# Optimization experiments

Measured on AMD Instinct MI355X. Metric: run time of the kernel, lower is better.

Reference implementation:

```python
import jax, jax.numpy as jnp
import numpy as np
from jax import lax

NUM_MELS = 80
NQ = 256          # num_quants
WIN = 1024
HOP = 256
K_UP = 800        # upsample kernel
PAD_UP = K_UP + 4 * HOP - WIN   # = 800
RC = 120          # residual_channels
SC = 240          # skip_channels
KC = 2            # causal kernel
NB = 16           # num blocks
DILS = [1, 2, 4, 8, 16, 32, 64, 128] * 2
DN = ('NCH', 'OIH', 'NCH')


def conv1x1(x, w, b):
    # x: [B,C,T], w: [O,C], b: [O]
    return jnp.einsum('bct,oc->bot', x, w) + b[None, :, None]


def causal_conv(x, w, b, d):
    # x: [B,RC,T], w: [2RC,RC,KC], left-pad by d*(KC-1) -> causal, same length
    y = lax.conv_general_dilated(x, w, (1,), [(d * (KC - 1), 0)],
                                 rhs_dilation=(d,), dimension_numbers=DN)
    return y + b[None, :, None]


def setup_inputs() -> dict:
    key = jax.random.key(0)
    ks = jax.random.split(key, 20)
    s = 0.05
    n = jax.random.normal
    return {
        'waveforms': n(ks[0], (1, 40960), jnp.float32),
        'melspecs': n(ks[1], (1, NUM_MELS, 160), jnp.float32),
        # ConvTranspose-equivalent upsample weight, stored as direct conv weight [O,I,K]
        'up_w': s * n(ks[2], (NUM_MELS, NUM_MELS, K_UP), jnp.float32),
        'up_b': jnp.zeros((NUM_MELS,), jnp.float32),
        'in_w': s * n(ks[3], (RC, 1), jnp.float32),
        'in_b': jnp.zeros((RC,), jnp.float32),
        'blk_causal_w': s * n(ks[4], (NB, 2 * RC, RC, KC), jnp.float32),
        'blk_causal_b': jnp.zeros((NB, 2 * RC), jnp.float32),
        'blk_cond_w': s * n(ks[5], (NB, 2 * RC, NUM_MELS), jnp.float32),
        'blk_cond_b': jnp.zeros((NB, 2 * RC), jnp.float32),
        'blk_skip_w': s * n(ks[6], (NB, SC, RC), jnp.float32),
        'blk_skip_b': jnp.zeros((NB, SC), jnp.float32),
        'blk_res_w': s * n(ks[7], (NB, RC, RC), jnp.float32),
        'blk_res_b': jnp.zeros((NB, RC), jnp.float32),
        'h1_w': s * n(ks[8], (NQ, SC), jnp.float32),
        'h1_b': jnp.zeros((NQ,), jnp.float32),
        'h2_w': s * n(ks[9], (NQ, NQ), jnp.float32),
        'h2_b': jnp.zeros((NQ,), jnp.float32),
    }


def _forward(waveforms, melspecs, up_w, up_b, in_w, in_b,
             blk_causal_w, blk_causal_b, blk_cond_w, blk_cond_b,
             blk_skip_w, blk_skip_b, blk_res_w, blk_res_b,
             h1_w, h1_b, h2_w, h2_b):
    # ConvTranspose1d(stride=HOP, padding=PAD_UP) as lhs-dilated conv:
    # out_len = (F-1)*HOP + K_UP - 2*PAD_UP
    cond = lax.conv_general_dilated(
        melspecs, up_w, (1,), [(K_UP - 1 - PAD_UP, K_UP - 1 - PAD_UP)],
        lhs_dilation=(HOP,), dimension_numbers=DN) + up_b[None, :, None]
    L = min(waveforms.shape[-1], cond.shape[-1])
    wav = waveforms[..., :L]
    cond = cond[..., :L]

    res = conv1x1(wav[:, None, :], in_w, in_b)          # [B,RC,L]
    skip_sum = jnp.zeros((res.shape[0], SC, L), res.dtype)
    for i, d in enumerate(DILS):
        z = causal_conv(res, blk_causal_w[i], blk_causal_b[i], d) \
            + conv1x1(cond, blk_cond_w[i], blk_cond_b[i])  # [B,2RC,L]
        h = jnp.tanh(z[:, :RC]) * jax.nn.sigmoid(z[:, RC:])
        skip_sum = skip_sum + conv1x1(h, blk_skip_w[i], blk_skip_b[i])
        res = res + conv1x1(h, blk_res_w[i], blk_res_b[i])

    x = jax.nn.relu(skip_sum)
    x = jax.nn.relu(conv1x1(x, h1_w, h1_b))
    logits = conv1x1(x, h2_w, h2_b)                      # [B,NQ,L]
    return logits


def reference(waveforms, melspecs, up_w, up_b, in_w, in_b,
              blk_causal_w, blk_causal_b, blk_cond_w, blk_cond_b,
              blk_skip_w, blk_skip_b, blk_res_w, blk_res_b,
              h1_w, h1_b, h2_w, h2_b):
    return _forward(waveforms, melspecs, up_w, up_b, in_w, in_b,
                    blk_causal_w, blk_causal_b, blk_cond_w, blk_cond_b,
                    blk_skip_w, blk_skip_b, blk_res_w, blk_res_b,
                    h1_w, h1_b, h2_w, h2_b)
```

## Files before the change

### kernel.cpp

```cpp
#include <hip/hip_runtime.h>

#define L_LEN 39904
#define NT 624
#define RCH 120
#define SCH 240
#define CMEL 80
#define NQO 256
#define NBLK 16
#define KUP 800

typedef unsigned short u16;
typedef __attribute__((ext_vector_type(8))) short short8;
typedef __attribute__((ext_vector_type(4))) float f32x4;

#define MFMA(a, b, c) __builtin_amdgcn_mfma_f32_16x16x32_bf16((a), (b), (c), 0, 0, 0)

__device__ __forceinline__ u16 f2bf(float f) {
    unsigned u = __float_as_uint(f);
    u += 0x7FFFu + ((u >> 16) & 1u);
    return (u16)(u >> 16);
}
__device__ __forceinline__ unsigned pack2(float a, float b) {
    return (unsigned)f2bf(a) | ((unsigned)f2bf(b) << 16);
}
__device__ __forceinline__ float b16tof(u16 h) {
    return __uint_as_float((unsigned)h << 16);
}
__device__ __forceinline__ float gate(float a, float b) {
    float ea = __expf(2.f * a);
    float th = 1.f - 2.f * __builtin_amdgcn_rcpf(ea + 1.f);
    float sg = __builtin_amdgcn_rcpf(1.f + __expf(-b));
    return th * sg;
}

constexpr size_t O_CONDT = 0;
constexpr size_t O_RESA  = O_CONDT + 7023104;
constexpr size_t O_RESB  = O_RESA + 19153920;
constexpr size_t O_SKIP  = O_RESB + 19153920;
constexpr size_t O_ZFRAG = O_SKIP + 19153920;
constexpr size_t O_SKF   = O_ZFRAG + 2621440;
constexpr size_t O_RF    = O_SKF + 1048576;
constexpr size_t O_H1F   = O_RF + 524288;
constexpr size_t O_H2F   = O_H1F + 131072;
constexpr size_t O_UPF   = O_H2F + 131072;
constexpr size_t O_ZB    = O_UPF + 13107200;
constexpr size_t O_SKB   = O_ZB + 16384;

constexpr size_t H2_CONDT = 0;
constexpr size_t H2_RESF  = 7023104;
constexpr size_t H2_BFA   = H2_RESF + 19153920;
constexpr size_t H2_BFB   = H2_BFA + 9576960;
constexpr size_t H2_ZFRAG = H2_BFB + 9576960;
constexpr size_t H2_SKF   = H2_ZFRAG + 2621440;
constexpr size_t H2_RF    = H2_SKF + 1048576;
constexpr size_t H2_H1F   = H2_RF + 524288;
constexpr size_t H2_H2F   = H2_H1F + 131072;
constexpr size_t H2_ZB    = H2_H2F + 131072;
constexpr size_t H2_SKBS  = H2_ZB + 16384;
constexpr size_t H2_HALL  = H2_SKBS + 16384;
constexpr size_t H_BYTES  = (size_t)NBLK * L_LEN * 120 * 2;
constexpr size_t UPF_BYTES = 13107200;
constexpr size_t NEED_H = H2_HALL + (H_BYTES > UPF_BYTES ? H_BYTES : UPF_BYTES);

__global__ void k_prep_zfrag(const float* __restrict__ bc_w, const float* __restrict__ bq_w,
                             u16* __restrict__ dst) {
    int i = blockIdx.x * 256 + threadIdx.x;
    if (i >= NBLK * 10 * 16 * 512) return;
    int jj = i & 7, lane = (i >> 3) & 63, mt = (i >> 9) & 15;
    int rest = i >> 13, ks = rest % 10, blk = rest / 10;
    int m = mt * 16 + (lane & 15);
    int k = ks * 32 + ((lane >> 4) << 3) + jj;
    float v = 0.f;
    if (m < 240) {
        int o = (m & 1) ? (m >> 1) + 120 : (m >> 1);
        if (k < 120)       v = bc_w[((size_t)(blk * 240 + o) * 120 + k) * 2 + 0];
        else if (k < 240)  v = bc_w[((size_t)(blk * 240 + o) * 120 + (k - 120)) * 2 + 1];
        else               v = bq_w[(size_t)(blk * 240 + o) * 80 + (k - 240)];
    }
    dst[i] = f2bf(v);
}
__global__ void k_prep_skfrag(const float* __restrict__ bs_w, u16* __restrict__ dst) {
    int i = blockIdx.x * 256 + threadIdx.x;
    if (i >= NBLK * 4 * 16 * 512) return;
    int jj = i & 7, lane = (i >> 3) & 63, mt = (i >> 9) & 15;
    int rest = i >> 13, ks = rest & 3, blk = rest >> 2;
    int m = mt * 16 + (lane & 15);
    int k = ks * 32 + ((lane >> 4) << 3) + jj;
    float v = (m < 240 && k < 120) ? bs_w[(size_t)(blk * 240 + m) * 120 + k] : 0.f;
    dst[i] = f2bf(v);
}
__global__ void k_prep_rfrag(const float* __restrict__ br_w, u16* __restrict__ dst) {
    int i = blockIdx.x * 256 + threadIdx.x;
    if (i >= NBLK * 4 * 8 * 512) return;
    int jj = i & 7, lane = (i >> 3) & 63, mt = (i >> 9) & 7;
    int rest = i >> 12, ks = rest & 3, blk = rest >> 2;
    int m = mt * 16 + (lane & 15);
    int k = ks * 32 + ((lane >> 4) << 3) + jj;
    float v = (m < 120 && k < 120) ? br_w[(size_t)(blk * 120 + m) * 120 + k] : 0.f;
    dst[i] = f2bf(v);
}
__global__ void k_prep_h1frag(const float* __restrict__ h1_w, u16* __restrict__ dst) {
    int i = blockIdx.x * 256 + threadIdx.x;
    if (i >= 8 * 16 * 512) return;
    int jj = i & 7, lane = (i >> 3) & 63, mt = (i >> 9) & 15, ks = i >> 13;
    int m = mt * 16 + (lane & 15);
    int k = ks * 32 + ((lane >> 4) << 3) + jj;
    float v = (k < 240) ? h1_w[(size_t)m * 240 + k] : 0.f;
    dst[i] = f2bf(v);
}
__global__ void k_prep_h2frag(const float* __restrict__ h2_w, u16* __restrict__ dst) {
    int i = blockIdx.x * 256 + threadIdx.x;
    if (i >= 8 * 16 * 512) return;
    int jj = i & 7, lane = (i >> 3) & 63, mt = (i >> 9) & 15, ks = i >> 13;
    int m = mt * 16 + (lane & 15);
    int k = ks * 32 + ((lane >> 4) << 3) + jj;
    dst[i] = f2bf(h2_w[(size_t)m * 256 + k]);
}
__global__ void k_prep_upfrag(const float* __restrict__ up_w, u16* __restrict__ dst) {
    int i = blockIdx.x * 256 + threadIdx.x;
    if (i >= 256 * 10 * 5 * 512) return;
    int jj = i & 7, lane = (i >> 3) & 63;
    int rest = i >> 9;
    int mt = rest % 5; rest /= 5;
    int ks = rest % 10; int p = rest / 10;
    int m = mt * 16 + (lane & 15);
    int k = ks * 32 + ((lane >> 4) << 3) + jj;
    int c = k >> 2, j = k & 3;
    int r = (256 - ((p + 1) & 255)) & 255;
    int kk = r + 256 * j;
    float v = (m < 80 && kk < KUP) ? up_w[((size_t)m * 80 + c) * KUP + kk] : 0.f;
    dst[i] = f2bf(v);
}
__global__ void k_prep_zbias(const float* __restrict__ bc_b, const float* __restrict__ bq_b,
                             float* __restrict__ dst) {
    int i = blockIdx.x * 256 + threadIdx.x;
    if (i >= NBLK * 256) return;
    int m = i & 255, blk = i >> 8;
    float v = 0.f;
    if (m < 240) {
        int o = (m & 1) ? (m >> 1) + 120 : (m >> 1);
        v = bc_b[blk * 240 + o] + bq_b[blk * 240 + o];
    }
    dst[i] = v;
}
__global__ void k_prep_skbias(const float* __restrict__ bs_b, float* __restrict__ dst) {
    int i = blockIdx.x * 256 + threadIdx.x;
    if (i >= NBLK * 240) return;
    dst[i] = bs_b[i];
}
__global__ void k_prep_skbsum(const float* __restrict__ bs_b, float* __restrict__ dst) {
    int m = blockIdx.x * 256 + threadIdx.x;
    if (m >= 240) return;
    float s = 0.f;
    for (int i = 0; i < NBLK; i++) s += bs_b[i * 240 + m];
    dst[m] = s;
}
__global__ void k_res_initT(const float* __restrict__ wav, const float* __restrict__ in_w,
                            const float* __restrict__ in_b, float* __restrict__ resT) {
    int i = blockIdx.x * 256 + threadIdx.x;
    if (i >= L_LEN * RCH) return;
    int t = i / RCH, c = i % RCH;
    resT[i] = wav[t] * in_w[c] + in_b[c];
}
__global__ void k_res_initTb(const float* __restrict__ wav, const float* __restrict__ in_w,
                             const float* __restrict__ in_b, u16* __restrict__ resB) {
    int i = blockIdx.x * 256 + threadIdx.x;
    if (i >= L_LEN * RCH) return;
    int t = i / RCH, c = i % RCH;
    resB[i] = f2bf(wav[t] * in_w[c] + in_b[c]);
}

__global__ __launch_bounds__(256) void k_up(const float* __restrict__ mel,
        const u16* __restrict__ upf, const float* __restrict__ up_b,
        u16* __restrict__ condT) {
    __shared__ u16 s_ms[64 * 328];
    const int tid = threadIdx.x, l = tid & 63, w = tid >> 6;
    const int quad = l >> 4, tloc = l & 15;
    const int p = blockIdx.x, s0 = blockIdx.y * 64;
    for (int rr = 0; rr < 16; rr++) {
        int tt = w + 4 * rr;
        int sg = s0 + tt;
        #pragma unroll
        for (int base = 0; base < 320; base += 64) {
            int ck = base + l;
            int c = ck >> 2, j = ck & 3;
            int mi = 1 + j + sg;
            float v = (mi < 160) ? mel[c * 160 + mi] : 0.f;
            s_ms[tt * 328 + ck] = f2bf(v);
        }
    }
    __syncthreads();
    f32x4 acc[2][4];
    #pragma unroll
    for (int i = 0; i < 2; i++)
        #pragma unroll
        for (int n = 0; n < 4; n++) acc[i][n] = (f32x4){0.f, 0.f, 0.f, 0.f};
    const int nmt = (w == 0) ? 2 : 1;
    int mts[2]; mts[0] = w; mts[1] = 4;
    for (int ks = 0; ks < 10; ks++) {
        short8 b[4];
        int k0 = ks * 32 + quad * 8;
        #pragma unroll
        for (int n = 0; n < 4; n++)
            b[n] = *(const short8*)&s_ms[(n * 16 + tloc) * 328 + k0];
        const short8* ap = (const short8*)(upf) + ((size_t)p * 10 + ks) * 5 * 64;
        for (int i = 0; i < nmt; i++) {
            short8 a = ap[mts[i] * 64 + l];
            #pragma unroll
            for (int n = 0; n < 4; n++) acc[i][n] = MFMA(a, b[n], acc[i][n]);
        }
    }
    for (int i = 0; i < nmt; i++) {
        int o_base = mts[i] * 16 + quad * 4;
        float4 ub = *(const float4*)(up_b + o_base);
        float bb[4] = {ub.x, ub.y, ub.z, ub.w};
        #pragma unroll
        for (int n = 0; n < 4; n++) {
            int sg = s0 + n * 16 + tloc;
            int t = p + 256 * sg;
            if (t < L_LEN) {
                #pragma unroll
                for (int r = 0; r < 4; r++)
                    condT[(size_t)t * 88 + o_base + r] = f2bf(acc[i][n][r] + bb[r]);
            }
        }
    }
}

__global__ __launch_bounds__(512, 4) void k_block(
        const u16* __restrict__ condT, const float* __restrict__ resT_in,
        float* __restrict__ resT_out, u16* __restrict__ skipT,
        const u16* __restrict__ zfrag, const u16* __restrict__ skfrag,
        const u16* __restrict__ rfrag, const float* __restrict__ zbias,
        const float* __restrict__ skbias, const float* __restrict__ resb,
        int blk, int dil, int first) {
    __shared__ u16 s_x[64 * 328];
    u16* s_h = s_x;
    const int tid = threadIdx.x, l = tid & 63, w = tid >> 6;
    const int quad = l >> 4, tloc = l & 15;
    const int t0 = blockIdx.x * 64;
    const short8* zap = (const short8*)(zfrag) + (size_t)blk * 10 * 16 * 64;
    short8 a_cur[2], a_nxt[2];
    #pragma unroll
    for (int i = 0; i < 2; i++) a_cur[i] = zap[(size_t)(w * 2 + i) * 64 + l];
    for (int rr = 0; rr < 8; rr++) {
        int tt = w + 8 * rr;
        int tg = t0 + tt, tp = tg - dil;
        if (l < 60) {
            float2 pv = make_float2(0.f, 0.f), cv = make_float2(0.f, 0.f);
            if (tp >= 0 && tp < L_LEN) pv = *(const float2*)(resT_in + (size_t)tp * 120 + 2 * l);
            if (tg < L_LEN)            cv = *(const float2*)(resT_in + (size_t)tg * 120 + 2 * l);
            *(unsigned*)&s_x[tt * 328 + 2 * l]       = pack2(pv.x, pv.y);
// ... 86 lines not shown
            ra_n = rap[((size_t)(ks + 1) * 8 + w) * 64 + l];
        }
        short8 b[4];
        int k0 = ks * 32 + quad * 8;
        #pragma unroll
        for (int n = 0; n < 4; n++)
            b[n] = *(const short8*)&s_h[(n * 16 + tloc) * 136 + k0];
        #pragma unroll
        for (int i = 0; i < 2; i++)
            #pragma unroll
            for (int n = 0; n < 4; n++) sacc[i][n] = MFMA(sa_c[i], b[n], sacc[i][n]);
        #pragma unroll
        for (int n = 0; n < 4; n++) racc[n] = MFMA(ra_c, b[n], racc[n]);
        #pragma unroll
        for (int i = 0; i < 2; i++) sa_c[i] = sa_n[i];
        ra_c = ra_n;
    }
    #pragma unroll
    for (int i = 0; i < 2; i++) {
        int m_base = (w * 2 + i) * 16 + quad * 4;
        if (m_base >= 240) continue;
        float4 sb4 = *(const float4*)(skbias + blk * 240 + m_base);
        #pragma unroll
        for (int n = 0; n < 4; n++) {
            int t = t0 + n * 16 + tloc;
            if (t >= L_LEN) continue;
            float x0 = sacc[i][n][0] + sb4.x;
            float x1 = sacc[i][n][1] + sb4.y;
            float x2 = sacc[i][n][2] + sb4.z;
            float x3 = sacc[i][n][3] + sb4.w;
            if (!first) {
                uint2 pv = skp[i][n];
                x0 += b16tof((u16)(pv.x & 0xFFFF));
                x1 += b16tof((u16)(pv.x >> 16));
                x2 += b16tof((u16)(pv.y & 0xFFFF));
                x3 += b16tof((u16)(pv.y >> 16));
            }
            uint2 ov;
            ov.x = pack2(x0, x1);
            ov.y = pack2(x2, x3);
            *(uint2*)(skipT + (size_t)t * 240 + m_base) = ov;
        }
    }
    {
        int m_base = w * 16 + quad * 4;
        if (m_base < 120) {
            float4 rb4 = *(const float4*)(resb + blk * 120 + m_base);
            #pragma unroll
            for (int n = 0; n < 4; n++) {
                int t = t0 + n * 16 + tloc;
                if (t >= L_LEN) continue;
                float4 cur = *(const float4*)(resT_in + (size_t)t * 120 + m_base);
                float4 o;
                o.x = cur.x + racc[n][0] + rb4.x;
                o.y = cur.y + racc[n][1] + rb4.y;
                o.z = cur.z + racc[n][2] + rb4.z;
                o.w = cur.w + racc[n][3] + rb4.w;
                *(float4*)(resT_out + (size_t)t * 120 + m_base) = o;
            }
        }
    }
}

__global__ __launch_bounds__(512, 4) void k_block_h4(
        const u16* __restrict__ condT,
        const u16* __restrict__ bfIn, u16* __restrict__ bfOut,
        u16* __restrict__ hout,
        const u16* __restrict__ zfrag, const u16* __restrict__ rfrag,
        const float* __restrict__ zbias, const float* __restrict__ resb,
        int blk, int dil) {
    __shared__ u16 s_x[64 * 328];
    u16* s_h = s_x;
    const int tid = threadIdx.x, l = tid & 63, w = tid >> 6;
    const int quad = l >> 4, tloc = l & 15;
    const int t0 = blockIdx.x * 64;
    const short8* zap = (const short8*)(zfrag) + (size_t)blk * 10 * 16 * 64;
    short8 a_cur[2], a_nxt[2];
    a_cur[0] = zap[(size_t)(w * 2 + 0) * 64 + l];
    a_cur[1] = zap[(size_t)(w * 2 + 1) * 64 + l];
    const uint2 Z2 = make_uint2(0u, 0u);
    for (int rr = 0; rr < 8; rr++) {
        int tt = w + 8 * rr, tg = t0 + tt;
        if (l < 30) {
            uint2 cv = (tg < L_LEN) ? *(const uint2*)(bfIn + (size_t)tg * 120 + 4 * l) : Z2;
            *(uint2*)&s_x[tt * 328 + 120 + 4 * l] = cv;
            if (tt < dil) {
                int tp = tg - dil;
                uint2 pv = (tp >= 0 && tp < L_LEN)
                    ? *(const uint2*)(bfIn + (size_t)tp * 120 + 4 * l) : Z2;
                *(uint2*)&s_x[tt * 328 + 4 * l] = pv;
            }
        } else if (l >= 32 && l < 54) {
            int c = l - 32;
            uint2 q = (tg < L_LEN) ? *(const uint2*)(condT + (size_t)tg * 88 + 4 * c) : Z2;
            *(uint2*)&s_x[tt * 328 + 240 + 4 * c] = q;
        }
    }
    __syncthreads();
    if (dil < 64) {
        for (int rr = 0; rr < 8; rr++) {
            int tt = w + 8 * rr;
            if (l < 30 && tt >= dil)
                *(uint2*)&s_x[tt * 328 + 4 * l] =
                    *(const uint2*)&s_x[(tt - dil) * 328 + 120 + 4 * l];
        }
        __syncthreads();
    }
    f32x4 acc[2][4];
    #pragma unroll
    for (int i = 0; i < 2; i++)
        #pragma unroll
        for (int n = 0; n < 4; n++) acc[i][n] = (f32x4){0.f, 0.f, 0.f, 0.f};
    for (int ks = 0; ks < 10; ks++) {
        if (ks < 9) {
            a_nxt[0] = zap[((size_t)(ks + 1) * 16 + w * 2 + 0) * 64 + l];
            a_nxt[1] = zap[((size_t)(ks + 1) * 16 + w * 2 + 1) * 64 + l];
        }
        int k0 = ks * 32 + quad * 8;
        short8 b[4];
        #pragma unroll
        for (int n = 0; n < 4; n++)
            b[n] = *(const short8*)&s_x[(n * 16 + tloc) * 328 + k0];
        #pragma unroll
        for (int i = 0; i < 2; i++)
            #pragma unroll
            for (int n = 0; n < 4; n++) acc[i][n] = MFMA(a_cur[i], b[n], acc[i][n]);
        a_cur[0] = a_nxt[0]; a_cur[1] = a_nxt[1];
    }
    const short8* rap = (const short8*)(rfrag) + (size_t)blk * 4 * 8 * 64;
    short8 ra_c = rap[(size_t)w * 64 + l], ra_n;
    const int m_r = w * 16 + quad * 4;
    uint2 curb[4];
    if (m_r < 120) {
        #pragma unroll
        for (int n = 0; n < 4; n++)
            curb[n] = *(const uint2*)&s_x[(n * 16 + tloc) * 328 + 120 + m_r];
    }
    unsigned hu[2][4];
    #pragma unroll
    for (int i = 0; i < 2; i++) {
        int m_base = (w * 2 + i) * 16 + quad * 4;
        float4 bz4 = *(const float4*)(zbias + blk * 256 + m_base);
        #pragma unroll
        for (int n = 0; n < 4; n++) {
            float h0 = gate(acc[i][n][0] + bz4.x, acc[i][n][1] + bz4.y);
            float h1 = gate(acc[i][n][2] + bz4.z, acc[i][n][3] + bz4.w);
            hu[i][n] = pack2(h0, h1);
        }
    }
    __syncthreads();
    #pragma unroll
    for (int i = 0; i < 2; i++) {
        int j0 = (w * 2 + i) * 8 + quad * 2;
        #pragma unroll
        for (int n = 0; n < 4; n++)
            *(unsigned*)&s_h[(n * 16 + tloc) * 136 + j0] = hu[i][n];
    }
    __syncthreads();
    for (int rr = 0; rr < 8; rr++) {
        int tt = w + 8 * rr, tg = t0 + tt;
        if (l < 60 && tg < L_LEN)
            *(unsigned*)&hout[(size_t)tg * 120 + 2 * l] =
                *(const unsigned*)&s_h[tt * 136 + 2 * l];
    }
    f32x4 racc[4];
    #pragma unroll
    for (int n = 0; n < 4; n++) racc[n] = (f32x4){0.f, 0.f, 0.f, 0.f};
    for (int ks = 0; ks < 4; ks++) {
        if (ks < 3) ra_n = rap[((size_t)(ks + 1) * 8 + w) * 64 + l];
        short8 b[4];
        int k0 = ks * 32 + quad * 8;
        #pragma unroll
        for (int n = 0; n < 4; n++)
            b[n] = *(const short8*)&s_h[(n * 16 + tloc) * 136 + k0];
        #pragma unroll
        for (int n = 0; n < 4; n++) racc[n] = MFMA(ra_c, b[n], racc[n]);
        ra_c = ra_n;
    }
    if (m_r < 120) {
        float4 rb4 = *(const float4*)(resb + blk * 120 + m_r);
        #pragma unroll
        for (int n = 0; n < 4; n++) {
            int t = t0 + n * 16 + tloc;
            if (t >= L_LEN) continue;
            float o0 = b16tof((u16)(curb[n].x & 0xFFFF)) + racc[n][0] + rb4.x;
            float o1 = b16tof((u16)(curb[n].x >> 16))    + racc[n][1] + rb4.y;
            float o2 = b16tof((u16)(curb[n].y & 0xFFFF)) + racc[n][2] + rb4.z;
            float o3 = b16tof((u16)(curb[n].y >> 16))    + racc[n][3] + rb4.w;
            uint2 hv;
            hv.x = pack2(o0, o1);
            hv.y = pack2(o2, o3);
            *(uint2*)(bfOut + (size_t)t * 120 + m_r) = hv;
        }
    }
}

__global__ __launch_bounds__(512, 4) void k_block_g4(
        const u16* __restrict__ condT,
        const u16* __restrict__ bfIn, u16* __restrict__ bfOut,
        u16* __restrict__ hall,
        const u16* __restrict__ zfrag, const u16* __restrict__ rfrag,
        const float* __restrict__ zbias, const float* __restrict__ resb,
        int base) {
    __shared__ u16 s_res[80 * 120];
    __shared__ u16 s_cond[80 * 88];
    __shared__ u16 s_h[80 * 136];
    const int tid = threadIdx.x, l = tid & 63, w = tid >> 6;
    const int quad = l >> 4, tloc = l & 15;
    const int t0 = blockIdx.x * 64;
    const uint2 Z2 = make_uint2(0u, 0u);
    for (int rr = 0; rr < 10; rr++) {
        int row = w + 8 * rr;
        int tg = t0 - 16 + row;
        bool ok = (tg >= 0 && tg < L_LEN);
        if (l < 30) {
            uint2 v = ok ? *(const uint2*)(bfIn + (size_t)tg * 120 + 4 * l) : Z2;
            *(uint2*)&s_res[row * 120 + 4 * l] = v;
        } else if (l >= 32 && l < 54) {
            int c = l - 32;
            uint2 q = ok ? *(const uint2*)(condT + (size_t)tg * 88 + 4 * c) : Z2;
            *(uint2*)&s_cond[row * 88 + 4 * c] = q;
        }
    }
    __syncthreads();
    const int m_r = w * 16 + quad * 4;
    for (int k = 0; k < 4; k++) {
        const int blk = base + k;
        const int d = 1 << k;
        const short8* zap = (const short8*)(zfrag) + (size_t)blk * 10 * 16 * 64;
        const short8* rap = (const short8*)(rfrag) + (size_t)blk * 4 * 8 * 64;
        u16* hout = hall + (size_t)blk * ((size_t)L_LEN * 120);
        short8 a_cur[2], a_nxt[2];
        a_cur[0] = zap[(size_t)(w * 2 + 0) * 64 + l];
        a_cur[1] = zap[(size_t)(w * 2 + 1) * 64 + l];
        f32x4 acc[2][5];
        #pragma unroll
        for (int i = 0; i < 2; i++)
            #pragma unroll
            for (int n = 0; n < 5; n++) acc[i][n] = (f32x4){0.f, 0.f, 0.f, 0.f};
        for (int ks = 0; ks < 10; ks++) {
            if (ks < 9) {
                a_nxt[0] = zap[((size_t)(ks + 1) * 16 + w * 2 + 0) * 64 + l];
                a_nxt[1] = zap[((size_t)(ks + 1) * 16 + w * 2 + 1) * 64 + l];
            }
            int k0 = ks * 32 + quad * 8;
            short8 b[5];
            #pragma unroll
            for (int n = 0; n < 5; n++) {
                int r = n * 16 + tloc;
                const u16* src;
                if (k0 < 120) {
                    int pr = r - d; if (pr < 0) pr = 0;
                    src = &s_res[pr * 120 + k0];
                } else if (k0 < 240) {
                    src = &s_res[r * 120 + (k0 - 120)];
                } else {
                    src = &s_cond[r * 88 + (k0 - 240)];
                }
                b[n] = *(const short8*)src;
            }
            #pragma unroll
            for (int i = 0; i < 2; i++)
                #pragma unroll
                for (int n = 0; n < 5; n++) acc[i][n] = MFMA(a_cur[i], b[n], acc[i][n]);
            a_cur[0] = a_nxt[0]; a_cur[1] = a_nxt[1];
        }
        unsigned hu[2][5];
        #pragma unroll
        for (int i = 0; i < 2; i++) {
            int m_base = (w * 2 + i) * 16 + quad * 4;
            float4 bz4 = *(const float4*)(zbias + blk * 256 + m_base);
            #pragma unroll
            for (int n = 0; n < 5; n++) {
                float h0 = gate(acc[i][n][0] + bz4.x, acc[i][n][1] + bz4.y);
                float h1 = gate(acc[i][n][2] + bz4.z, acc[i][n][3] + bz4.w);
                hu[i][n] = pack2(h0, h1);
            }
        }
        #pragma unroll
        for (int i = 0; i < 2; i++) {
            int j0 = (w * 2 + i) * 8 + quad * 2;
            #pragma unroll
            for (int n = 0; n < 5; n++)
                *(unsigned*)&s_h[(n * 16 + tloc) * 136 + j0] = hu[i][n];
        }
        __syncthreads();
        for (int rr = 0; rr < 8; rr++) {
            int row = 16 + w + 8 * rr;
            int tg = t0 + w + 8 * rr;
            if (l < 60 && tg < L_LEN)
                *(unsigned*)&hout[(size_t)tg * 120 + 2 * l] =
                    *(const unsigned*)&s_h[row * 136 + 2 * l];
        }
        f32x4 racc[5];
        #pragma unroll
        for (int n = 0; n < 5; n++) racc[n] = (f32x4){0.f, 0.f, 0.f, 0.f};
        short8 ra_c = rap[(size_t)w * 64 + l], ra_n;
        for (int ks = 0; ks < 4; ks++) {
            if (ks < 3) ra_n = rap[((size_t)(ks + 1) * 8 + w) * 64 + l];
            short8 b[5];
            int k0 = ks * 32 + quad * 8;
            #pragma unroll
            for (int n = 0; n < 5; n++)
                b[n] = *(const short8*)&s_h[(n * 16 + tloc) * 136 + k0];
            #pragma unroll
            for (int n = 0; n < 5; n++) racc[n] = MFMA(ra_c, b[n], racc[n]);
            ra_c = ra_n;
        }
        if (m_r < 120) {
            float4 rb4 = *(const float4*)(resb + blk * 120 + m_r);
            #pragma unroll
            for (int n = 0; n < 5; n++) {
                int row = n * 16 + tloc;
                int tg = t0 - 16 + row;
                if (tg < 0 || tg >= L_LEN) continue;
                uint2 cv = *(const uint2*)&s_res[row * 120 + m_r];
                float o0 = b16tof((u16)(cv.x & 0xFFFF)) + racc[n][0] + rb4.x;
                float o1 = b16tof((u16)(cv.x >> 16))    + racc[n][1] + rb4.y;
                float o2 = b16tof((u16)(cv.y & 0xFFFF)) + racc[n][2] + rb4.z;
                float o3 = b16tof((u16)(cv.y >> 16))    + racc[n][3] + rb4.w;
                uint2 hv;
                hv.x = pack2(o0, o1);
                hv.y = pack2(o2, o3);
                *(uint2*)&s_res[row * 120 + m_r] = hv;
            }
        }
        __syncthreads();
    }
    for (int rr = 0; rr < 8; rr++) {
        int row = 16 + w + 8 * rr;
        int tg = t0 + w + 8 * rr;
        if (l < 30 && tg < L_LEN)
            *(uint2*)(bfOut + (size_t)tg * 120 + 4 * l) =
                *(const uint2*)&s_res[row * 120 + 4 * l];
    }
}

__global__ __launch_bounds__(512, 4) void k_final(const u16* __restrict__ skipT,
        const u16* __restrict__ h1f, const u16* __restrict__ h2f,
        const float* __restrict__ h1_b, const float* __restrict__ h2_b,
        float* __restrict__ out) {
    __shared__ u16 s_m[64 * 264];
    const int tid = threadIdx.x, l = tid & 63, w = tid >> 6;
    const int quad = l >> 4, tloc = l & 15;
    const int t0 = blockIdx.x * 64;
    const short8* ap1 = (const short8*)h1f;
    short8 a_cur[2], a_nxt[2];
    #pragma unroll
    for (int i = 0; i < 2; i++) a_cur[i] = ap1[(size_t)(w * 2 + i) * 64 + l];
    for (int rr = 0; rr < 8; rr++) {
        int tt = w + 8 * rr;
        int tg = t0 + tt;
        uint2 v = make_uint2(0u, 0u);
        if (l < 60 && tg < L_LEN)
            v = *(const uint2*)(skipT + (size_t)tg * 240 + 4 * l);
        float x0 = fmaxf(b16tof((u16)(v.x & 0xFFFF)), 0.f);
        float x1 = fmaxf(b16tof((u16)(v.x >> 16)), 0.f);
        float x2 = fmaxf(b16tof((u16)(v.y & 0xFFFF)), 0.f);
        float x3 = fmaxf(b16tof((u16)(v.y >> 16)), 0.f);
        uint2 ov;
        ov.x = pack2(x0, x1);
        ov.y = pack2(x2, x3);
        *(uint2*)&s_m[tt * 264 + 4 * l] = ov;
    }
    __syncthreads();
    f32x4 acc[2][4];
    #pragma unroll
    for (int i = 0; i < 2; i++)
        #pragma unroll
        for (int n = 0; n < 4; n++) acc[i][n] = (f32x4){0.f, 0.f, 0.f, 0.f};
    for (int ks = 0; ks < 8; ks++) {
        if (ks < 7) {
            #pragma unroll
            for (int i = 0; i < 2; i++)
                a_nxt[i] = ap1[((size_t)(ks + 1) * 16 + w * 2 + i) * 64 + l];
        }
        short8 b[4];
        int k0 = ks * 32 + quad * 8;
        #pragma unroll
        for (int n = 0; n < 4; n++)
            b[n] = *(const short8*)&s_m[(n * 16 + tloc) * 264 + k0];
        #pragma unroll
        for (int i = 0; i < 2; i++)
            #pragma unroll
            for (int n = 0; n < 4; n++) acc[i][n] = MFMA(a_cur[i], b[n], acc[i][n]);
        #pragma unroll
        for (int i = 0; i < 2; i++) a_cur[i] = a_nxt[i];
    }
    unsigned ylo[2][4], yhi[2][4];
    #pragma unroll
    for (int i = 0; i < 2; i++) {
        int m_base = (w * 2 + i) * 16 + quad * 4;
        float4 b1 = *(const float4*)(h1_b + m_base);
        #pragma unroll
        for (int n = 0; n < 4; n++) {
            float y0 = fmaxf(acc[i][n][0] + b1.x, 0.f);
            float y1v = fmaxf(acc[i][n][1] + b1.y, 0.f);
            float y2 = fmaxf(acc[i][n][2] + b1.z, 0.f);
            float y3 = fmaxf(acc[i][n][3] + b1.w, 0.f);
            ylo[i][n] = pack2(y0, y1v);
            yhi[i][n] = pack2(y2, y3);
        }
    }
    const short8* ap2 = (const short8*)h2f;
    #pragma unroll
    for (int i = 0; i < 2; i++) a_cur[i] = ap2[(size_t)(w * 2 + i) * 64 + l];
    __syncthreads();
    #pragma unroll
    for (int i = 0; i < 2; i++) {
        int m_base = (w * 2 + i) * 16 + quad * 4;
        #pragma unroll
        for (int n = 0; n < 4; n++) {
            int t = n * 16 + tloc;
            *(unsigned*)&s_m[t * 264 + m_base]     = ylo[i][n];
            *(unsigned*)&s_m[t * 264 + m_base + 2] = yhi[i][n];
        }
    }
    __syncthreads();
    #pragma unroll
    for (int i = 0; i < 2; i++)
        #pragma unroll
        for (int n = 0; n < 4; n++) acc[i][n] = (f32x4){0.f, 0.f, 0.f, 0.f};
    for (int ks = 0; ks < 8; ks++) {
        if (ks < 7) {
            #pragma unroll
            for (int i = 0; i < 2; i++)
                a_nxt[i] = ap2[((size_t)(ks + 1) * 16 + w * 2 + i) * 64 + l];
        }
        short8 b[4];
        int k0 = ks * 32 + quad * 8;
        #pragma unroll
        for (int n = 0; n < 4; n++)
            b[n] = *(const short8*)&s_m[(n * 16 + tloc) * 264 + k0];
        #pragma unroll
        for (int i = 0; i < 2; i++)
            #pragma unroll
            for (int n = 0; n < 4; n++) acc[i][n] = MFMA(a_cur[i], b[n], acc[i][n]);
        #pragma unroll
        for (int i = 0; i < 2; i++) a_cur[i] = a_nxt[i];
    }
    #pragma unroll
    for (int i = 0; i < 2; i++) {
        int m_base = (w * 2 + i) * 16 + quad * 4;
        float4 b2 = *(const float4*)(h2_b + m_base);
        float bb[4] = {b2.x, b2.y, b2.z, b2.w};
        #pragma unroll
        for (int n = 0; n < 4; n++) {
            int t = t0 + n * 16 + tloc;
            if (t >= L_LEN) continue;
            #pragma unroll
            for (int r = 0; r < 4; r++)
                out[(size_t)(m_base + r) * L_LEN + t] = acc[i][n][r] + bb[r];
        }
    }
}

__global__ __launch_bounds__(512, 4) void k_final_h3(const u16* __restrict__ hall,
        const u16* __restrict__ skf, const u16* __restrict__ h1f,
        const u16* __restrict__ h2f, const float* __restrict__ skbsum,
        const float* __restrict__ h1_b, const float* __restrict__ h2_b,
        float* __restrict__ out) {
    __shared__ u16 smem[2 * 64 * 136];
    u16* s_m = smem;
    const int tid = threadIdx.x, l = tid & 63, w = tid >> 6;
    const int quad = l >> 4, tloc = l & 15;
    const int t0 = blockIdx.x * 64;
    const short8* sap = (const short8*)skf;

    unsigned ha[8], hb[8];
    auto LOADH = [&](unsigned (&reg)[8], int i) {
        const u16* hp = hall + (size_t)i * ((size_t)L_LEN * 120);
        #pragma unroll
        for (int rr = 0; rr < 8; rr++) {
            int tg = t0 + w + 8 * rr;
            reg[rr] = (l < 60 && tg < L_LEN)
                ? *(const unsigned*)&hp[(size_t)tg * 120 + 2 * l] : 0u;
        }
    };
    if (l >= 60) {
        #pragma unroll
        for (int rr = 0; rr < 8; rr++) {
            int row = w + 8 * rr;
            *(unsigned*)&smem[row * 136 + 2 * l] = 0u;
            *(unsigned*)&smem[64 * 136 + row * 136 + 2 * l] = 0u;
        }
    }
    LOADH(ha, 0);
    #pragma unroll
    for (int rr = 0; rr < 8; rr++)
        if (l < 60) *(unsigned*)&smem[(w + 8 * rr) * 136 + 2 * l] = ha[rr];
    LOADH(hb, 1);
    short8 sa_c[2], sa_n[2];
    sa_c[0] = sap[(size_t)(w * 2 + 0) * 64 + l];
    sa_c[1] = sap[(size_t)(w * 2 + 1) * 64 + l];
    f32x4 sacc[2][4];
    #pragma unroll
    for (int i = 0; i < 2; i++)
        #pragma unroll
        for (int n = 0; n < 4; n++) sacc[i][n] = (f32x4){0.f, 0.f, 0.f, 0.f};
    __syncthreads();
    #pragma unroll
    for (int i = 0; i < 16; i++) {
        u16* cur = smem + (i & 1) * (64 * 136);
        u16* nxt = smem + ((i + 1) & 1) * (64 * 136);
        unsigned (&wrg)[8] = (i & 1) ? ha : hb;
        unsigned (&lrg)[8] = (i & 1) ? hb : ha;
        if (i < 15) {
            #pragma unroll
            for (int rr = 0; rr < 8; rr++)
                if (l < 60) *(unsigned*)&nxt[(w + 8 * rr) * 136 + 2 * l] = wrg[rr];
        }
        if (i < 14) LOADH(lrg, i + 2);
        for (int ks = 0; ks < 4; ks++) {
            int g = i * 4 + ks;
            if (g < 63) {
                sa_n[0] = sap[((size_t)(g + 1) * 16 + w * 2 + 0) * 64 + l];
                sa_n[1] = sap[((size_t)(g + 1) * 16 + w * 2 + 1) * 64 + l];
            }
            int k0 = ks * 32 + quad * 8;
            short8 b[4];
            #pragma unroll
            for (int n = 0; n < 4; n++)
                b[n] = *(const short8*)&cur[(n * 16 + tloc) * 136 + k0];
            #pragma unroll
            for (int i2 = 0; i2 < 2; i2++)
                #pragma unroll
                for (int n = 0; n < 4; n++)
                    sacc[i2][n] = MFMA(sa_c[i2], b[n], sacc[i2][n]);
            sa_c[0] = sa_n[0]; sa_c[1] = sa_n[1];
        }
        __syncthreads();
    }
    const short8* ap1 = (const short8*)h1f;
    short8 a_cur[2], a_nxt[2];
    a_cur[0] = ap1[(size_t)(w * 2 + 0) * 64 + l];
    a_cur[1] = ap1[(size_t)(w * 2 + 1) * 64 + l];
    #pragma unroll
    for (int i2 = 0; i2 < 2; i2++) {
        int m_base = (w * 2 + i2) * 16 + quad * 4;
        float4 sb4 = make_float4(0.f, 0.f, 0.f, 0.f);
        bool valid = (m_base < 240);
        if (valid) sb4 = *(const float4*)(skbsum + m_base);
        #pragma unroll
        for (int n = 0; n < 4; n++) {
            float x0 = 0.f, x1 = 0.f, x2 = 0.f, x3 = 0.f;
            if (valid) {
                x0 = fmaxf(sacc[i2][n][0] + sb4.x, 0.f);
                x1 = fmaxf(sacc[i2][n][1] + sb4.y, 0.f);
                x2 = fmaxf(sacc[i2][n][2] + sb4.z, 0.f);
                x3 = fmaxf(sacc[i2][n][3] + sb4.w, 0.f);
            }
            int t = n * 16 + tloc;
            *(unsigned*)&s_m[t * 264 + m_base]     = pack2(x0, x1);
            *(unsigned*)&s_m[t * 264 + m_base + 2] = pack2(x2, x3);
        }
    }
    __syncthreads();
    f32x4 acc[2][4];
    #pragma unroll
    for (int i = 0; i < 2; i++)
        #pragma unroll
        for (int n = 0; n < 4; n++) acc[i][n] = (f32x4){0.f, 0.f, 0.f, 0.f};
    for (int ks = 0; ks < 8; ks++) {
        if (ks < 7) {
            #pragma unroll
            for (int i = 0; i < 2; i++)
                a_nxt[i] = ap1[((size_t)(ks + 1) * 16 + w * 2 + i) * 64 + l];
        }
        short8 b[4];
        int k0 = ks * 32 + quad * 8;
        #pragma unroll
        for (int n = 0; n < 4; n++)
            b[n] = *(const short8*)&s_m[(n * 16 + tloc) * 264 + k0];
        #pragma unroll
        for (int i = 0; i < 2; i++)
            #pragma unroll
            for (int n = 0; n < 4; n++) acc[i][n] = MFMA(a_cur[i], b[n], acc[i][n]);
        #pragma unroll
        for (int i = 0; i < 2; i++) a_cur[i] = a_nxt[i];
    }
    unsigned ylo[2][4], yhi[2][4];
    #pragma unroll
    for (int i = 0; i < 2; i++) {
        int m_base = (w * 2 + i) * 16 + quad * 4;
        float4 b1 = *(const float4*)(h1_b + m_base);
        #pragma unroll
        for (int n = 0; n < 4; n++) {
            float y0 = fmaxf(acc[i][n][0] + b1.x, 0.f);
            float y1v = fmaxf(acc[i][n][1] + b1.y, 0.f);
            float y2 = fmaxf(acc[i][n][2] + b1.z, 0.f);
            float y3 = fmaxf(acc[i][n][3] + b1.w, 0.f);
            ylo[i][n] = pack2(y0, y1v);
            yhi[i][n] = pack2(y2, y3);
        }
    }
    const short8* ap2 = (const short8*)h2f;
    #pragma unroll
    for (int i = 0; i < 2; i++) a_cur[i] = ap2[(size_t)(w * 2 + i) * 64 + l];
    __syncthreads();
    #pragma unroll
    for (int i = 0; i < 2; i++) {
        int m_base = (w * 2 + i) * 16 + quad * 4;
        #pragma unroll
        for (int n = 0; n < 4; n++) {
            int t = n * 16 + tloc;
            *(unsigned*)&s_m[t * 264 + m_base]     = ylo[i][n];
            *(unsigned*)&s_m[t * 264 + m_base + 2] = yhi[i][n];
        }
    }
    __syncthreads();
    #pragma unroll
    for (int i = 0; i < 2; i++)
        #pragma unroll
        for (int n = 0; n < 4; n++) acc[i][n] = (f32x4){0.f, 0.f, 0.f, 0.f};
    for (int ks = 0; ks < 8; ks++) {
        if (ks < 7) {
            #pragma unroll
            for (int i = 0; i < 2; i++)
                a_nxt[i] = ap2[((size_t)(ks + 1) * 16 + w * 2 + i) * 64 + l];
        }
        short8 b[4];
        int k0 = ks * 32 + quad * 8;
        #pragma unroll
        for (int n = 0; n < 4; n++)
            b[n] = *(const short8*)&s_m[(n * 16 + tloc) * 264 + k0];
        #pragma unroll
        for (int i = 0; i < 2; i++)
            #pragma unroll
            for (int n = 0; n < 4; n++) acc[i][n] = MFMA(a_cur[i], b[n], acc[i][n]);
        #pragma unroll
        for (int i = 0; i < 2; i++) a_cur[i] = a_nxt[i];
    }
    #pragma unroll
    for (int i = 0; i < 2; i++) {
        int m_base = (w * 2 + i) * 16 + quad * 4;
        float4 b2 = *(const float4*)(h2_b + m_base);
        float bb[4] = {b2.x, b2.y, b2.z, b2.w};
        #pragma unroll
        for (int n = 0; n < 4; n++) {
            int t = t0 + n * 16 + tloc;
            if (t >= L_LEN) continue;
            #pragma unroll
            for (int r = 0; r < 4; r++)
                out[(size_t)(m_base + r) * L_LEN + t] = acc[i][n][r] + bb[r];
        }
    }
}

extern "C" void kernel_launch(void* const* d_in, const int* in_sizes, int n_in,
                              void* d_out, int out_size, void* d_ws, size_t ws_size,
                              hipStream_t stream) {
    const float* wav   = (const float*)d_in[0];
    const float* mel   = (const float*)d_in[1];
    const float* up_w  = (const float*)d_in[2];
    const float* up_b  = (const float*)d_in[3];
    const float* in_w  = (const float*)d_in[4];
    const float* in_b  = (const float*)d_in[5];
    const float* bc_w  = (const float*)d_in[6];
    const float* bc_b  = (const float*)d_in[7];
    const float* bq_w  = (const float*)d_in[8];
    const float* bq_b  = (const float*)d_in[9];
    const float* bs_w  = (const float*)d_in[10];
    const float* bs_b  = (const float*)d_in[11];
    const float* br_w  = (const float*)d_in[12];
    const float* br_b  = (const float*)d_in[13];
    const float* h1_w  = (const float*)d_in[14];
    const float* h1_b  = (const float*)d_in[15];
    const float* h2_w  = (const float*)d_in[16];
    const float* h2_b  = (const float*)d_in[17];

    char* wsb = (char*)d_ws;
    const bool use_h = (ws_size >= NEED_H);

    if (use_h) {
        u16*   condT = (u16*)(wsb + H2_CONDT);
        u16*   bfA   = (u16*)(wsb + H2_BFA);
        u16*   bfB   = (u16*)(wsb + H2_BFB);
        u16*   zfrag = (u16*)(wsb + H2_ZFRAG);
        u16*   skf   = (u16*)(wsb + H2_SKF);
        u16*   rf    = (u16*)(wsb + H2_RF);
        u16*   h1f   = (u16*)(wsb + H2_H1F);
        u16*   h2f   = (u16*)(wsb + H2_H2F);
        float* zb    = (float*)(wsb + H2_ZB);
        float* skbs  = (float*)(wsb + H2_SKBS);
        u16*   hall  = (u16*)(wsb + H2_HALL);
        u16*   upf   = (u16*)(wsb + H2_HALL);

        k_prep_zfrag <<<5120, 256, 0, stream>>>(bc_w, bq_w, zfrag);
        k_prep_skfrag<<<2048, 256, 0, stream>>>(bs_w, skf);
        k_prep_rfrag <<<1024, 256, 0, stream>>>(br_w, rf);
        k_prep_h1frag<<<256, 256, 0, stream>>>(h1_w, h1f);
        k_prep_h2frag<<<256, 256, 0, stream>>>(h2_w, h2f);
        k_prep_upfrag<<<25600, 256, 0, stream>>>(up_w, upf);
        k_prep_zbias <<<16, 256, 0, stream>>>(bc_b, bq_b, zb);
        k_prep_skbsum<<<1, 256, 0, stream>>>(bs_b, skbs);
        k_res_initTb <<<(L_LEN * RCH + 255) / 256, 256, 0, stream>>>(wav, in_w, in_b, bfA);
        k_up<<<dim3(256, 3), 256, 0, stream>>>(mel, upf, up_b, condT);

        u16* rin = bfA;
        u16* rout = bfB;
        k_block_g4<<<NT, 512, 0, stream>>>(condT, rin, rout, hall, zfrag, rf, zb, br_b, 0);
        { u16* t = rin; rin = rout; rout = t; }
        for (int i = 4; i < 8; i++) {
            k_block_h4<<<NT, 512, 0, stream>>>(condT, rin, rout,
                                               hall + (size_t)i * (size_t)L_LEN * 120,
                                               zfrag, rf, zb, br_b, i, 1 << (i & 7));
            u16* t = rin; rin = rout; rout = t;
        }
        k_block_g4<<<NT, 512, 0, stream>>>(condT, rin, rout, hall, zfrag, rf, zb, br_b, 8);
        { u16* t = rin; rin = rout; rout = t; }
        for (int i = 12; i < 16; i++) {
            k_block_h4<<<NT, 512, 0, stream>>>(condT, rin, rout,
                                               hall + (size_t)i * (size_t)L_LEN * 120,
                                               zfrag, rf, zb, br_b, i, 1 << (i & 7));
            u16* t = rin; rin = rout; rout = t;
        }
        k_final_h3<<<NT, 512, 0, stream>>>(hall, skf, h1f, h2f, skbs, h1_b, h2_b,
                                           (float*)d_out);
    } else {
        u16*   condT = (u16*)(wsb + O_CONDT);
        float* resA  = (float*)(wsb + O_RESA);
        float* resB  = (float*)(wsb + O_RESB);
        u16*   skipT = (u16*)(wsb + O_SKIP);
        u16*   zfrag = (u16*)(wsb + O_ZFRAG);
        u16*   skf   = (u16*)(wsb + O_SKF);
        u16*   rf    = (u16*)(wsb + O_RF);
        u16*   h1f   = (u16*)(wsb + O_H1F);
        u16*   h2f   = (u16*)(wsb + O_H2F);
        u16*   upf   = (u16*)(wsb + O_UPF);
        float* zb    = (float*)(wsb + O_ZB);
        float* skb   = (float*)(wsb + O_SKB);

        k_prep_zfrag <<<5120, 256, 0, stream>>>(bc_w, bq_w, zfrag);
        k_prep_skfrag<<<2048, 256, 0, stream>>>(bs_w, skf);
        k_prep_rfrag <<<1024, 256, 0, stream>>>(br_w, rf);
        k_prep_h1frag<<<256, 256, 0, stream>>>(h1_w, h1f);
        k_prep_h2frag<<<256, 256, 0, stream>>>(h2_w, h2f);
        k_prep_upfrag<<<25600, 256, 0, stream>>>(up_w, upf);
        k_prep_zbias <<<16, 256, 0, stream>>>(bc_b, bq_b, zb);
        k_prep_skbias<<<15, 256, 0, stream>>>(bs_b, skb);
        k_res_initT  <<<(L_LEN * RCH + 255) / 256, 256, 0, stream>>>(wav, in_w, in_b, resA);
        k_up<<<dim3(256, 3), 256, 0, stream>>>(mel, upf, up_b, condT);

        for (int i = 0; i < NBLK; i++) {
            int d = 1 << (i & 7);
            const float* rin = (i & 1) ? resB : resA;
            float* rout      = (i & 1) ? resA : resB;
            k_block<<<NT, 512, 0, stream>>>(condT, rin, rout, skipT, zfrag, skf, rf,
                                            zb, skb, br_b, i, d, (i == 0) ? 1 : 0);
        }
        k_final<<<NT, 512, 0, stream>>>(skipT, h1f, h2f, h1_b, h2_b, (float*)d_out);
    }
}
```

Measured before the change: 704.9 us.

## Fuse five dilation blocks per group kernel and pad activation rows to 128

```diff
diff --git a/kernel.cpp b/kernel.cpp
--- a/kernel.cpp
+++ b/kernel.cpp
@@ -46,21 +46,20 @@
 constexpr size_t O_ZB    = O_UPF + 13107200;
 constexpr size_t O_SKB   = O_ZB + 16384;
 
-constexpr size_t H2_CONDT = 0;
-constexpr size_t H2_RESF  = 7023104;
-constexpr size_t H2_BFA   = H2_RESF + 19153920;
-constexpr size_t H2_BFB   = H2_BFA + 9576960;
-constexpr size_t H2_ZFRAG = H2_BFB + 9576960;
-constexpr size_t H2_SKF   = H2_ZFRAG + 2621440;
-constexpr size_t H2_RF    = H2_SKF + 1048576;
-constexpr size_t H2_H1F   = H2_RF + 524288;
-constexpr size_t H2_H2F   = H2_H1F + 131072;
-constexpr size_t H2_ZB    = H2_H2F + 131072;
-constexpr size_t H2_SKBS  = H2_ZB + 16384;
-constexpr size_t H2_HALL  = H2_SKBS + 16384;
-constexpr size_t H_BYTES  = (size_t)NBLK * L_LEN * 120 * 2;
+constexpr size_t H3_CONDT = 0;
+constexpr size_t H3_BFA   = 7023104;
+constexpr size_t H3_BFB   = H3_BFA + 10215424;
+constexpr size_t H3_ZFRAG = H3_BFB + 10215424;
+constexpr size_t H3_SKF   = H3_ZFRAG + 2621440;
+constexpr size_t H3_RF    = H3_SKF + 1048576;
+constexpr size_t H3_H1F   = H3_RF + 524288;
+constexpr size_t H3_H2F   = H3_H1F + 131072;
+constexpr size_t H3_ZB    = H3_H2F + 131072;
+constexpr size_t H3_SKBS  = H3_ZB + 16384;
+constexpr size_t H3_HALL  = H3_SKBS + 16384;
+constexpr size_t H_BYTES  = (size_t)NBLK * L_LEN * 128 * 2;
 constexpr size_t UPF_BYTES = 13107200;
-constexpr size_t NEED_H = H2_HALL + (H_BYTES > UPF_BYTES ? H_BYTES : UPF_BYTES);
+constexpr size_t NEED_H = H3_HALL + (H_BYTES > UPF_BYTES ? H_BYTES : UPF_BYTES);
 
 __global__ void k_prep_zfrag(const float* __restrict__ bc_w, const float* __restrict__ bq_w,
                              u16* __restrict__ dst) {
@@ -165,9 +164,10 @@
 __global__ void k_res_initTb(const float* __restrict__ wav, const float* __restrict__ in_w,
                              const float* __restrict__ in_b, u16* __restrict__ resB) {
     int i = blockIdx.x * 256 + threadIdx.x;
-    if (i >= L_LEN * RCH) return;
-    int t = i / RCH, c = i % RCH;
-    resB[i] = f2bf(wav[t] * in_w[c] + in_b[c]);
+    if (i >= L_LEN * 128) return;
+    int t = i >> 7, c = i & 127;
+    float v = (c < 120) ? (wav[t] * in_w[c] + in_b[c]) : 0.f;
+    resB[i] = f2bf(v);
 }
 
 __global__ __launch_bounds__(256) void k_up(const float* __restrict__ mel,
@@ -420,12 +420,12 @@
     for (int rr = 0; rr < 8; rr++) {
         int tt = w + 8 * rr, tg = t0 + tt;
         if (l < 30) {
-            uint2 cv = (tg < L_LEN) ? *(const uint2*)(bfIn + (size_t)tg * 120 + 4 * l) : Z2;
+            uint2 cv = (tg < L_LEN) ? *(const uint2*)(bfIn + (size_t)tg * 128 + 4 * l) : Z2;
             *(uint2*)&s_x[tt * 328 + 120 + 4 * l] = cv;
             if (tt < dil) {
                 int tp = tg - dil;
                 uint2 pv = (tp >= 0 && tp < L_LEN)
-                    ? *(const uint2*)(bfIn + (size_t)tp * 120 + 4 * l) : Z2;
+                    ? *(const uint2*)(bfIn + (size_t)tp * 128 + 4 * l) : Z2;
                 *(uint2*)&s_x[tt * 328 + 4 * l] = pv;
             }
         } else if (l >= 32 && l < 54) {
@@ -497,8 +497,8 @@
     __syncthreads();
     for (int rr = 0; rr < 8; rr++) {
         int tt = w + 8 * rr, tg = t0 + tt;
-        if (l < 60 && tg < L_LEN)
-            *(unsigned*)&hout[(size_t)tg * 120 + 2 * l] =
+        if (tg < L_LEN)
+            *(unsigned*)&hout[(size_t)tg * 128 + 2 * l] =
                 *(const unsigned*)&s_h[tt * 136 + 2 * l];
     }
     f32x4 racc[4];
@@ -528,31 +528,31 @@
             uint2 hv;
             hv.x = pack2(o0, o1);
             hv.y = pack2(o2, o3);
-            *(uint2*)(bfOut + (size_t)t * 120 + m_r) = hv;
-        }
-    }
-}
-
-__global__ __launch_bounds__(512, 4) void k_block_g4(
+            *(uint2*)(bfOut + (size_t)t * 128 + m_r) = hv;
+        }
+    }
+}
+
+__global__ __launch_bounds__(512, 4) void k_block_g5(
         const u16* __restrict__ condT,
         const u16* __restrict__ bfIn, u16* __restrict__ bfOut,
         u16* __restrict__ hall,
         const u16* __restrict__ zfrag, const u16* __restrict__ rfrag,
         const float* __restrict__ zbias, const float* __restrict__ resb,
         int base) {
-    __shared__ u16 s_res[80 * 120];
-    __shared__ u16 s_cond[80 * 88];
-    __shared__ u16 s_h[80 * 136];
+    __shared__ u16 s_res[96 * 120];
+    __shared__ u16 s_cond[96 * 88];
+    __shared__ u16 s_h[96 * 132];
     const int tid = threadIdx.x, l = tid & 63, w = tid >> 6;
     const int quad = l >> 4, tloc = l & 15;
     const int t0 = blockIdx.x * 64;
     const uint2 Z2 = make_uint2(0u, 0u);
-    for (int rr = 0; rr < 10; rr++) {
+    for (int rr = 0; rr < 12; rr++) {
         int row = w + 8 * rr;
-        int tg = t0 - 16 + row;
+        int tg = t0 - 32 + row;
         bool ok = (tg >= 0 && tg < L_LEN);
         if (l < 30) {
-            uint2 v = ok ? *(const uint2*)(bfIn + (size_t)tg * 120 + 4 * l) : Z2;
+            uint2 v = ok ? *(const uint2*)(bfIn + (size_t)tg * 128 + 4 * l) : Z2;
             *(uint2*)&s_res[row * 120 + 4 * l] = v;
         } else if (l >= 32 && l < 54) {
             int c = l - 32;
@@ -562,29 +562,29 @@
     }
     __syncthreads();
     const int m_r = w * 16 + quad * 4;
-    for (int k = 0; k < 4; k++) {
+    for (int k = 0; k < 5; k++) {
         const int blk = base + k;
         const int d = 1 << k;
         const short8* zap = (const short8*)(zfrag) + (size_t)blk * 10 * 16 * 64;
         const short8* rap = (const short8*)(rfrag) + (size_t)blk * 4 * 8 * 64;
-        u16* hout = hall + (size_t)blk * ((size_t)L_LEN * 120);
+        u16* hout = hall + (size_t)blk * ((size_t)L_LEN * 128);
         short8 a_cur[2], a_nxt[2];
         a_cur[0] = zap[(size_t)(w * 2 + 0) * 64 + l];
         a_cur[1] = zap[(size_t)(w * 2 + 1) * 64 + l];
-        f32x4 acc[2][5];
+        f32x4 acc[2][6];
         #pragma unroll
         for (int i = 0; i < 2; i++)
             #pragma unroll
-            for (int n = 0; n < 5; n++) acc[i][n] = (f32x4){0.f, 0.f, 0.f, 0.f};
+            for (int n = 0; n < 6; n++) acc[i][n] = (f32x4){0.f, 0.f, 0.f, 0.f};
         for (int ks = 0; ks < 10; ks++) {
             if (ks < 9) {
                 a_nxt[0] = zap[((size_t)(ks + 1) * 16 + w * 2 + 0) * 64 + l];
                 a_nxt[1] = zap[((size_t)(ks + 1) * 16 + w * 2 + 1) * 64 + l];
             }
             int k0 = ks * 32 + quad * 8;
-            short8 b[5];
-            #pragma unroll
-            for (int n = 0; n < 5; n++) {
+            short8 b[6];
+            #pragma unroll
+            for (int n = 0; n < 6; n++) {
                 int r = n * 16 + tloc;
                 const u16* src;
                 if (k0 < 120) {
@@ -600,16 +600,16 @@
             #pragma unroll
             for (int i = 0; i < 2; i++)
                 #pragma unroll
-                for (int n = 0; n < 5; n++) acc[i][n] = MFMA(a_cur[i], b[n], acc[i][n]);
+                for (int n = 0; n < 6; n++) acc[i][n] = MFMA(a_cur[i], b[n], acc[i][n]);
             a_cur[0] = a_nxt[0]; a_cur[1] = a_nxt[1];
         }
-        unsigned hu[2][5];
+        unsigned hu[2][6];
         #pragma unroll
         for (int i = 0; i < 2; i++) {
             int m_base = (w * 2 + i) * 16 + quad * 4;
             float4 bz4 = *(const float4*)(zbias + blk * 256 + m_base);
             #pragma unroll
-            for (int n = 0; n < 5; n++) {
+            for (int n = 0; n < 6; n++) {
                 float h0 = gate(acc[i][n][0] + bz4.x, acc[i][n][1] + bz4.y);
                 float h1 = gate(acc[i][n][2] + bz4.z, acc[i][n][3] + bz4.w);
                 hu[i][n] = pack2(h0, h1);
@@ -619,38 +619,38 @@
         for (int i = 0; i < 2; i++) {
             int j0 = (w * 2 + i) * 8 + quad * 2;
             #pragma unroll
-            for (int n = 0; n < 5; n++)
-                *(unsigned*)&s_h[(n * 16 + tloc) * 136 + j0] = hu[i][n];
+            for (int n = 0; n < 6; n++)
+                *(unsigned*)&s_h[(n * 16 + tloc) * 132 + j0] = hu[i][n];
         }
         __syncthreads();
         for (int rr = 0; rr < 8; rr++) {
-            int row = 16 + w + 8 * rr;
+            int row = 32 + w + 8 * rr;
             int tg = t0 + w + 8 * rr;
-            if (l < 60 && tg < L_LEN)
-                *(unsigned*)&hout[(size_t)tg * 120 + 2 * l] =
-                    *(const unsigned*)&s_h[row * 136 + 2 * l];
-        }
-        f32x4 racc[5];
-        #pragma unroll
-        for (int n = 0; n < 5; n++) racc[n] = (f32x4){0.f, 0.f, 0.f, 0.f};
+            if (tg < L_LEN)
+                *(unsigned*)&hout[(size_t)tg * 128 + 2 * l] =
+                    *(const unsigned*)&s_h[row * 132 + 2 * l];
+        }
+        f32x4 racc[6];
+        #pragma unroll
+        for (int n = 0; n < 6; n++) racc[n] = (f32x4){0.f, 0.f, 0.f, 0.f};
         short8 ra_c = rap[(size_t)w * 64 + l], ra_n;
         for (int ks = 0; ks < 4; ks++) {
             if (ks < 3) ra_n = rap[((size_t)(ks + 1) * 8 + w) * 64 + l];
-            short8 b[5];
+            short8 b[6];
             int k0 = ks * 32 + quad * 8;
             #pragma unroll
-            for (int n = 0; n < 5; n++)
-                b[n] = *(const short8*)&s_h[(n * 16 + tloc) * 136 + k0];
-            #pragma unroll
-            for (int n = 0; n < 5; n++) racc[n] = MFMA(ra_c, b[n], racc[n]);
+            for (int n = 0; n < 6; n++)
+                b[n] = *(const short8*)&s_h[(n * 16 + tloc) * 132 + k0];
+            #pragma unroll
+            for (int n = 0; n < 6; n++) racc[n] = MFMA(ra_c, b[n], racc[n]);
             ra_c = ra_n;
         }
         if (m_r < 120) {
             float4 rb4 = *(const float4*)(resb + blk * 120 + m_r);
             #pragma unroll
-            for (int n = 0; n < 5; n++) {
+            for (int n = 0; n < 6; n++) {
                 int row = n * 16 + tloc;
-                int tg = t0 - 16 + row;
+                int tg = t0 - 32 + row;
                 if (tg < 0 || tg >= L_LEN) continue;
                 uint2 cv = *(const uint2*)&s_res[row * 120 + m_r];
                 float o0 = b16tof((u16)(cv.x & 0xFFFF)) + racc[n][0] + rb4.x;
@@ -666,11 +666,15 @@
         __syncthreads();
     }
     for (int rr = 0; rr < 8; rr++) {
-        int row = 16 + w + 8 * rr;
+        int row = 32 + w + 8 * rr;
         int tg = t0 + w + 8 * rr;
-        if (l < 30 && tg < L_LEN)
-            *(uint2*)(bfOut + (size_t)tg * 120 + 4 * l) =
-                *(const uint2*)&s_res[row * 120 + 4 * l];
+        if (tg < L_LEN) {
+            if (l < 30)
+                *(uint2*)(bfOut + (size_t)tg * 128 + 4 * l) =
+                    *(const uint2*)&s_res[row * 120 + 4 * l];
+            else if (l < 32)
+                *(uint2*)(bfOut + (size_t)tg * 128 + 4 * l) = Z2;
+        }
     }
 }
 
@@ -807,26 +811,18 @@
 
     unsigned ha[8], hb[8];
     auto LOADH = [&](unsigned (&reg)[8], int i) {
-        const u16* hp = hall + (size_t)i * ((size_t)L_LEN * 120);
+        const u16* hp = hall + (size_t)i * ((size_t)L_LEN * 128);
         #pragma unroll
         for (int rr = 0; rr < 8; rr++) {
             int tg = t0 + w + 8 * rr;
-            reg[rr] = (l < 60 && tg < L_LEN)
-                ? *(const unsigned*)&hp[(size_t)tg * 120 + 2 * l] : 0u;
+            reg[rr] = (tg < L_LEN)
+                ? *(const unsigned*)&hp[(size_t)tg * 128 + 2 * l] : 0u;
         }
     };
-    if (l >= 60) {
-        #pragma unroll
-        for (int rr = 0; rr < 8; rr++) {
-            int row = w + 8 * rr;
-            *(unsigned*)&smem[row * 136 + 2 * l] = 0u;
-            *(unsigned*)&smem[64 * 136 + row * 136 + 2 * l] = 0u;
-        }
-    }
     LOADH(ha, 0);
     #pragma unroll
     for (int rr = 0; rr < 8; rr++)
-        if (l < 60) *(unsigned*)&smem[(w + 8 * rr) * 136 + 2 * l] = ha[rr];
+        *(unsigned*)&smem[(w + 8 * rr) * 136 + 2 * l] = ha[rr];
     LOADH(hb, 1);
     short8 sa_c[2], sa_n[2];
     sa_c[0] = sap[(size_t)(w * 2 + 0) * 64 + l];
@@ -846,7 +842,7 @@
         if (i < 15) {
             #pragma unroll
             for (int rr = 0; rr < 8; rr++)
-                if (l < 60) *(unsigned*)&nxt[(w + 8 * rr) * 136 + 2 * l] = wrg[rr];
+                *(unsigned*)&nxt[(w + 8 * rr) * 136 + 2 * l] = wrg[rr];
         }
         if (i < 14) LOADH(lrg, i + 2);
         for (int ks = 0; ks < 4; ks++) {
@@ -1011,18 +1007,18 @@
     const bool use_h = (ws_size >= NEED_H);
 
     if (use_h) {
-        u16*   condT = (u16*)(wsb + H2_CONDT);
-        u16*   bfA   = (u16*)(wsb + H2_BFA);
-        u16*   bfB   = (u16*)(wsb + H2_BFB);
-        u16*   zfrag = (u16*)(wsb + H2_ZFRAG);
-        u16*   skf   = (u16*)(wsb + H2_SKF);
-        u16*   rf    = (u16*)(wsb + H2_RF);
-        u16*   h1f   = (u16*)(wsb + H2_H1F);
-        u16*   h2f   = (u16*)(wsb + H2_H2F);
-        float* zb    = (float*)(wsb + H2_ZB);
-        float* skbs  = (float*)(wsb + H2_SKBS);
-        u16*   hall  = (u16*)(wsb + H2_HALL);
-        u16*   upf   = (u16*)(wsb + H2_HALL);
+        u16*   condT = (u16*)(wsb + H3_CONDT);
+        u16*   bfA   = (u16*)(wsb + H3_BFA);
+        u16*   bfB   = (u16*)(wsb + H3_BFB);
+        u16*   zfrag = (u16*)(wsb + H3_ZFRAG);
+        u16*   skf   = (u16*)(wsb + H3_SKF);
+        u16*   rf    = (u16*)(wsb + H3_RF);
+        u16*   h1f   = (u16*)(wsb + H3_H1F);
+        u16*   h2f   = (u16*)(wsb + H3_H2F);
+        float* zb    = (float*)(wsb + H3_ZB);
+        float* skbs  = (float*)(wsb + H3_SKBS);
+        u16*   hall  = (u16*)(wsb + H3_HALL);
+        u16*   upf   = (u16*)(wsb + H3_HALL);
 
         k_prep_zfrag <<<5120, 256, 0, stream>>>(bc_w, bq_w, zfrag);
         k_prep_skfrag<<<2048, 256, 0, stream>>>(bs_w, skf);
@@ -1032,24 +1028,24 @@
         k_prep_upfrag<<<25600, 256, 0, stream>>>(up_w, upf);
         k_prep_zbias <<<16, 256, 0, stream>>>(bc_b, bq_b, zb);
         k_prep_skbsum<<<1, 256, 0, stream>>>(bs_b, skbs);
-        k_res_initTb <<<(L_LEN * RCH + 255) / 256, 256, 0, stream>>>(wav, in_w, in_b, bfA);
+        k_res_initTb <<<(L_LEN * 128 + 255) / 256, 256, 0, stream>>>(wav, in_w, in_b, bfA);
         k_up<<<dim3(256, 3), 256, 0, stream>>>(mel, upf, up_b, condT);
 
         u16* rin = bfA;
         u16* rout = bfB;
-        k_block_g4<<<NT, 512, 0, stream>>>(condT, rin, rout, hall, zfrag, rf, zb, br_b, 0);
+        k_block_g5<<<NT, 512, 0, stream>>>(condT, rin, rout, hall, zfrag, rf, zb, br_b, 0);
         { u16* t = rin; rin = rout; rout = t; }
-        for (int i = 4; i < 8; i++) {
+        for (int i = 5; i < 8; i++) {
             k_block_h4<<<NT, 512, 0, stream>>>(condT, rin, rout,
-                                               hall + (size_t)i * (size_t)L_LEN * 120,
+                                               hall + (size_t)i * (size_t)L_LEN * 128,
                                                zfrag, rf, zb, br_b, i, 1 << (i & 7));
             u16* t = rin; rin = rout; rout = t;
         }
-        k_block_g4<<<NT, 512, 0, stream>>>(condT, rin, rout, hall, zfrag, rf, zb, br_b, 8);
+        k_block_g5<<<NT, 512, 0, stream>>>(condT, rin, rout, hall, zfrag, rf, zb, br_b, 8);
         { u16* t = rin; rin = rout; rout = t; }
-        for (int i = 12; i < 16; i++) {
+        for (int i = 13; i < 16; i++) {
             k_block_h4<<<NT, 512, 0, stream>>>(condT, rin, rout,
-                                               hall + (size_t)i * (size_t)L_LEN * 120,
+                                               hall + (size_t)i * (size_t)L_LEN * 128,
                                                zfrag, rf, zb, br_b, i, 1 << (i & 7));
             u16* t = rin; rin = rout; rout = t;
         }
```

Measured after the change: 821.9 us. 1.17x slower.
